# Kernel tuning notes

Measured on AMD Instinct MI355X. Metric: run time of the kernel, lower is better.

Reference implementation:

```python
import jax, jax.numpy as jnp
import numpy as np

N = 50000   # nodes (subjects in population graph)
E = 800000  # edges (similarity graph, avg degree 16)
F = 128     # node features


def setup_inputs() -> dict:
    key = jax.random.key(0)
    ks = jax.random.split(key, 8)

    def glorot(k, shape):
        scale = 1.0 / np.sqrt(shape[0])
        return jax.random.normal(k, shape, jnp.float32) * scale

    x = jax.random.normal(ks[0], (N, F), jnp.float32)
    edge_index = jax.random.randint(ks[1], (2, E), 0, N, dtype=jnp.int64)
    return {
        "x": x,
        "edge_index": edge_index,
        "W1": glorot(ks[2], (F, 128)),   "b1": jnp.zeros((128,), jnp.float32),
        "W2": glorot(ks[3], (128, 64)),  "b2": jnp.zeros((64,), jnp.float32),
        "Wf1": glorot(ks[4], (64, 32)),  "bf1": jnp.zeros((32,), jnp.float32),
        "Wf2": glorot(ks[5], (32, 1)),   "bf2": jnp.zeros((1,), jnp.float32),
    }


def reference(x, edge_index, W1, b1, W2, b2, Wf1, bf1, Wf2, bf2):
    n = x.shape[0]
    # GCNConv (PyG default): add self-loops, symmetric deg^{-1/2} normalization
    loops = jnp.arange(n, dtype=edge_index.dtype)
    src = jnp.concatenate([edge_index[0], loops])  # [E+N]
    dst = jnp.concatenate([edge_index[1], loops])  # [E+N]
    deg = jax.ops.segment_sum(jnp.ones_like(dst, x.dtype), dst, num_segments=n)
    dinv = deg ** -0.5  # deg >= 1 thanks to self-loops
    norm = (dinv[src] * dinv[dst])[:, None]  # [E+N, 1]

    def gcn_conv(h, W, b):
        h = h @ W                                    # transform [n, out]
        msg = h[src] * norm                          # gather + normalize
        agg = jax.ops.segment_sum(msg, dst, num_segments=n)  # scatter-add
        return agg + b

    h = jnp.tanh(gcn_conv(x, W1, b1))
    h = jnp.tanh(gcn_conv(h, W2, b2))
    h = jnp.tanh(h @ Wf1 + bf1)
    return h @ Wf2 + bf2  # [n, 1] brain-age prediction
```

## Files before the change

### kernel.cpp

```cpp
#include <hip/hip_runtime.h>
#include <hip/hip_fp16.h>
#include <math.h>

#define TPB 256
#define CAP 64

typedef int   nt_i4 __attribute__((ext_vector_type(4)));
typedef unsigned nt_u4 __attribute__((ext_vector_type(4)));
typedef _Float16 f16x8 __attribute__((ext_vector_type(8)));
typedef float f32x4 __attribute__((ext_vector_type(4)));

__global__ __launch_bounds__(TPB) void init_degi(const int* __restrict__ e,
                                                 int* __restrict__ flag,
                                                 int* __restrict__ degi, int n) {
  int i = blockIdx.x * TPB + threadIdx.x;
  const int stride = gridDim.x * TPB;
  for (; i < n; i += stride) degi[i] = 0;
  if (blockIdx.x == 0) {
    __shared__ int found;
    if (threadIdx.x == 0) found = 0;
    __syncthreads();
    int nz = 0;
    for (int k = threadIdx.x; k < 2048; k += TPB)
      nz |= (e[2 * k + 1] != 0) ? 1 : 0;
    if (nz) atomicOr(&found, 1);
    __syncthreads();
    if (threadIdx.x == 0) *flag = found;
  }
}

__device__ __forceinline__ void load_edge(const void* eptr, int flag, int E,
                                          int e, int& s, int& d) {
  if (flag) {
    const int* p = (const int*)eptr;
    s = p[e];
    d = p[E + e];
  } else {
    const long long* p = (const long long*)eptr;
    s = (int)p[e];
    d = (int)p[E + e];
  }
}

__global__ __launch_bounds__(TPB) void build_ell(const void* __restrict__ eptr,
                                                 const int* __restrict__ flag,
                                                 int* __restrict__ degi,
                                                 int* __restrict__ ell, int E) {
  const int fl = *flag;
  const int t4 = (blockIdx.x * TPB + threadIdx.x) * 4;
  const int stride = gridDim.x * TPB * 4;
  for (int e0 = t4; e0 < E; e0 += stride) {
    if (e0 + 4 <= E) {
      int s[4], d[4];
      if (fl) {
        const int* p = (const int*)eptr;
        nt_i4 sv = __builtin_nontemporal_load((const nt_i4*)&p[e0]);
        nt_i4 dv = __builtin_nontemporal_load((const nt_i4*)&p[E + e0]);
        s[0] = sv.x; s[1] = sv.y; s[2] = sv.z; s[3] = sv.w;
        d[0] = dv.x; d[1] = dv.y; d[2] = dv.z; d[3] = dv.w;
      } else {
        const long long* p = (const long long*)eptr;
        nt_i4 sa = __builtin_nontemporal_load((const nt_i4*)&p[e0]);
        nt_i4 sb = __builtin_nontemporal_load((const nt_i4*)&p[e0 + 2]);
        nt_i4 da = __builtin_nontemporal_load((const nt_i4*)&p[E + e0]);
        nt_i4 db = __builtin_nontemporal_load((const nt_i4*)&p[E + e0 + 2]);
        s[0] = sa.x; s[1] = sa.z; s[2] = sb.x; s[3] = sb.z;
        d[0] = da.x; d[1] = da.z; d[2] = db.x; d[3] = db.z;
      }
#pragma unroll
      for (int j = 0; j < 4; j++) {
        int slot = atomicAdd(&degi[d[j]], 1);
        if (slot < CAP)
          __builtin_nontemporal_store(s[j], &ell[(size_t)d[j] * CAP + slot]);
      }
    } else {
      for (int e = e0; e < E; e++) {
        int s, d;
        load_edge(eptr, fl, E, e, s, d);
        int slot = atomicAdd(&degi[d], 1);
        if (slot < CAP)
          __builtin_nontemporal_store(s, &ell[(size_t)d * CAP + slot]);
      }
    }
  }
}

template <int NC, typename AT>
__global__ __launch_bounds__(TPB, 4) void gemm_mfma(const AT* __restrict__ A,
                                                    const float* __restrict__ W,
                                                    const int* __restrict__ degi,
                                                    __half* __restrict__ out, int nrows) {
  constexpr int K = 128;
  constexpr int WT = 136;
  constexpr int NT = NC / 16;
  __shared__ _Float16 Wt[NC * WT];

  const int tid = threadIdx.x;

  for (int idx = tid; idx < NC * (K / 2); idx += TPB) {
    int c = idx % NC;
    int p = idx / NC;
    float w0 = W[(2 * p) * NC + c];
    float w1 = W[(2 * p + 1) * NC + c];
    __half2* dst = (__half2*)&Wt[c * WT + 2 * p];
    *dst = __floats2half2_rn(w0, w1);
  }
  __syncthreads();

  const int w = tid >> 6;
  const int lane = tid & 63;
  const int l15 = lane & 15;
  const int q = lane >> 4;
  const int m_base = blockIdx.x * 64 + w * 16;
  const int m = m_base + l15;
  const bool mok = m < nrows;

  f32x4 acc[NT];
#pragma unroll
  for (int t = 0; t < NT; t++) acc[t] = (f32x4){0.f, 0.f, 0.f, 0.f};

#pragma unroll
  for (int ks = 0; ks < 4; ks++) {
    const int k0 = ks * 32;
    f16x8 a;
    if (sizeof(AT) == 4) {
      float4 f0 = make_float4(0.f, 0.f, 0.f, 0.f), f1 = f0;
      if (mok) {
        const float* ap = (const float*)A + (size_t)m * K + k0 + q * 8;
        f0 = *(const float4*)ap;
        f1 = *(const float4*)(ap + 4);
      }
      a[0] = (_Float16)f0.x; a[1] = (_Float16)f0.y;
      a[2] = (_Float16)f0.z; a[3] = (_Float16)f0.w;
      a[4] = (_Float16)f1.x; a[5] = (_Float16)f1.y;
      a[6] = (_Float16)f1.z; a[7] = (_Float16)f1.w;
    } else {
      union { uint4 u; f16x8 h; } ld;
      ld.u = make_uint4(0, 0, 0, 0);
      if (mok)
        ld.u = *(const uint4*)((const __half*)A + (size_t)m * K + k0 + q * 8);
      a = ld.h;
    }
#pragma unroll
    for (int t = 0; t < NT; t++) {
      f16x8 b = *(const f16x8*)&Wt[(t * 16 + l15) * WT + k0 + q * 8];
      acc[t] = __builtin_amdgcn_mfma_f32_16x16x32_f16(a, b, acc[t], 0, 0, 0);
    }
  }

#pragma unroll
  for (int r = 0; r < 4; r++) {
    int row = m_base + q * 4 + r;
    if (row >= nrows) continue;
    float di = rsqrtf((float)(degi[row] + 1));
#pragma unroll
    for (int t = 0; t < NT; t++)
      out[(size_t)row * NC + t * 16 + l15] = (__half)(acc[t][r] * di);
  }
}

__global__ __launch_bounds__(TPB) void gcn_agg1_fused(const int* __restrict__ degi,
                                                      const int* __restrict__ ell,
                                                      const __half* __restrict__ t,
                                                      const float* __restrict__ bias,
                                                      const float* __restrict__ W2,
                                                      __half* __restrict__ t2, int n) {
  constexpr int NC = 128, LPN = 16, CPL = 8, NPB = TPB / LPN;
  constexpr int WT = 136;
  __shared__ _Float16 Wt2[64 * WT];
  __shared__ _Float16 Ah[NPB * WT];

  const int tid = threadIdx.x;

  for (int idx = tid; idx < 64 * 64; idx += TPB) {
    int c = idx & 63;
    int p = idx >> 6;
    float w0 = W2[(2 * p) * 64 + c];
    float w1 = W2[(2 * p + 1) * 64 + c];
    *(__half2*)&Wt2[c * WT + 2 * p] = __floats2half2_rn(w0, w1);
  }

  const int g = tid / LPN;
  const int ll = tid % LPN;
  const int node = blockIdx.x * NPB + g;
  const bool active = node < n;

  if (active) {
    int dg = degi[node];
    float di = rsqrtf((float)(dg + 1));
    int deg = dg > CAP ? CAP : dg;
    const int* nbr = &ell[(size_t)node * CAP];
    const __half* tp = t + (size_t)ll * CPL;

    float acc[CPL];
#pragma unroll
    for (int c = 0; c < CPL; c++) acc[c] = 0.f;

    union Ld { uint4 u4; __half2 h[4]; };
    auto addv = [&](const Ld& v) {
#pragma unroll
      for (int c = 0; c < 4; c++) {
        float2 f = __half22float2(v.h[c]);
        acc[2 * c] += f.x;
        acc[2 * c + 1] += f.y;
      }
    };

    int j = 0;
    for (; j + 8 <= deg; j += 8) {
      nt_i4 n0 = __builtin_nontemporal_load((const nt_i4*)&nbr[j]);
      nt_i4 n1 = __builtin_nontemporal_load((const nt_i4*)&nbr[j + 4]);
      Ld v0, v1, v2, v3, v4, v5, v6, v7;
      v0.u4 = *(const uint4*)&tp[(size_t)n0.x * NC];
      v1.u4 = *(const uint4*)&tp[(size_t)n0.y * NC];
      v2.u4 = *(const uint4*)&tp[(size_t)n0.z * NC];
      v3.u4 = *(const uint4*)&tp[(size_t)n0.w * NC];
      v4.u4 = *(const uint4*)&tp[(size_t)n1.x * NC];
      v5.u4 = *(const uint4*)&tp[(size_t)n1.y * NC];
      v6.u4 = *(const uint4*)&tp[(size_t)n1.z * NC];
      v7.u4 = *(const uint4*)&tp[(size_t)n1.w * NC];
      addv(v0); addv(v1); addv(v2); addv(v3);
      addv(v4); addv(v5); addv(v6); addv(v7);
    }
    for (; j + 4 <= deg; j += 4) {
      nt_i4 n0 = __builtin_nontemporal_load((const nt_i4*)&nbr[j]);
      Ld v0, v1, v2, v3;
      v0.u4 = *(const uint4*)&tp[(size_t)n0.x * NC];
      v1.u4 = *(const uint4*)&tp[(size_t)n0.y * NC];
      v2.u4 = *(const uint4*)&tp[(size_t)n0.z * NC];
      v3.u4 = *(const uint4*)&tp[(size_t)n0.w * NC];
      addv(v0); addv(v1); addv(v2); addv(v3);
    }
    for (; j < deg; j++) {
      Ld v;
      v.u4 = *(const uint4*)&tp[(size_t)nbr[j] * NC];
      addv(v);
    }
    {
      Ld v;
      v.u4 = *(const uint4*)&tp[(size_t)node * NC];
      addv(v);
    }

    const float* bp = &bias[ll * CPL];
    float bv[CPL];
#pragma unroll
    for (int c = 0; c < CPL; c += 4) {
      float4 b = *(const float4*)&bp[c];
      bv[c] = b.x; bv[c + 1] = b.y; bv[c + 2] = b.z; bv[c + 3] = b.w;
    }
    union { _Float16 h[8]; f16x8 v; } o;
#pragma unroll
    for (int c = 0; c < CPL; c++)
      o.h[c] = (_Float16)tanhf(acc[c] * di + bv[c]);
    *(f16x8*)&Ah[g * WT + ll * CPL] = o.v;
  }
  __syncthreads();

  const int w = tid >> 6;
  const int lane = tid & 63;
  const int l15 = lane & 15;
  const int q = lane >> 4;
  f32x4 acc2 = (f32x4){0.f, 0.f, 0.f, 0.f};
#pragma unroll
  for (int ks = 0; ks < 4; ks++) {
    f16x8 a = *(const f16x8*)&Ah[l15 * WT + ks * 32 + q * 8];
    f16x8 b = *(const f16x8*)&Wt2[(w * 16 + l15) * WT + ks * 32 + q * 8];
    acc2 = __builtin_amdgcn_mfma_f32_16x16x32_f16(a, b, acc2, 0, 0, 0);
  }
#pragma unroll
  for (int r = 0; r < 4; r++) {
    int rn = blockIdx.x * NPB + q * 4 + r;
    if (rn < n) {
      float d2 = rsqrtf((float)(degi[rn] + 1));
      t2[(size_t)rn * 64 + w * 16 + l15] = (__half)(acc2[r] * d2);
    }
  }
}

__global__ __launch_bounds__(TPB) void gcn_aggregate_head(
    const int* __restrict__ degi, const int* __restrict__ ell,
    const __half* __restrict__ t, const float* __restrict__ b2,
    const float* __restrict__ Wf1, const float* __restrict__ bf1,
    const float* __restrict__ Wf2, const float* __restrict__ bf2,
    float* __restrict__ out, int n) {
  constexpr int NC = 64, LPN = 16, NPB = TPB / LPN;
  __shared__ float hrow[NPB][68];
  __shared__ float Wf1s[64 * 32];
  __shared__ float Wf2s[32];
  const int tid = threadIdx.x;

#pragma unroll
  for (int i = 0; i < 2; i++) {
    int lid = tid + i * TPB;
    *(float4*)&Wf1s[lid * 4] = *(const float4*)&Wf1[lid * 4];
  }
  if (tid < 32) Wf2s[tid] = Wf2[tid];

  const int g = tid / LPN;
  const int ll = tid % LPN;
  const int node = blockIdx.x * NPB + g;
  const bool active = node < n;

  float acc[4] = {0.f, 0.f, 0.f, 0.f};
  if (active) {
    int dg = degi[node];
    float di = rsqrtf((float)(dg + 1));
    int deg = dg > CAP ? CAP : dg;
    const int* nbr = &ell[(size_t)node * CAP];
    const __half* tp = t + (size_t)ll * 4;
    union Ld { uint2 u2; __half2 h[2]; };
    auto addv = [&](const Ld& v) {
      float2 f0 = __half22float2(v.h[0]);
      float2 f1 = __half22float2(v.h[1]);
      acc[0] += f0.x; acc[1] += f0.y; acc[2] += f1.x; acc[3] += f1.y;
    };
    int j = 0;
    for (; j + 8 <= deg; j += 8) {
      nt_i4 n0 = __builtin_nontemporal_load((const nt_i4*)&nbr[j]);
      nt_i4 n1 = __builtin_nontemporal_load((const nt_i4*)&nbr[j + 4]);
      Ld v0, v1, v2, v3, v4, v5, v6, v7;
      v0.u2 = *(const uint2*)&tp[(size_t)n0.x * NC];
      v1.u2 = *(const uint2*)&tp[(size_t)n0.y * NC];
      v2.u2 = *(const uint2*)&tp[(size_t)n0.z * NC];
      v3.u2 = *(const uint2*)&tp[(size_t)n0.w * NC];
      v4.u2 = *(const uint2*)&tp[(size_t)n1.x * NC];
      v5.u2 = *(const uint2*)&tp[(size_t)n1.y * NC];
      v6.u2 = *(const uint2*)&tp[(size_t)n1.z * NC];
      v7.u2 = *(const uint2*)&tp[(size_t)n1.w * NC];
      addv(v0); addv(v1); addv(v2); addv(v3);
      addv(v4); addv(v5); addv(v6); addv(v7);
    }
    for (; j + 4 <= deg; j += 4) {
      nt_i4 nn = __builtin_nontemporal_load((const nt_i4*)&nbr[j]);
      Ld v0, v1, v2, v3;
      v0.u2 = *(const uint2*)&tp[(size_t)nn.x * NC];
      v1.u2 = *(const uint2*)&tp[(size_t)nn.y * NC];
      v2.u2 = *(const uint2*)&tp[(size_t)nn.z * NC];
      v3.u2 = *(const uint2*)&tp[(size_t)nn.w * NC];
      addv(v0); addv(v1); addv(v2); addv(v3);
    }
    for (; j < deg; j++) {
      Ld v;
      v.u2 = *(const uint2*)&tp[(size_t)nbr[j] * NC];
      addv(v);
    }
    {
      Ld v;
      v.u2 = *(const uint2*)&tp[(size_t)node * NC];
      addv(v);
    }
    float4 b = *(const float4*)&b2[ll * 4];
    hrow[g][ll * 4 + 0] = tanhf(acc[0] * di + b.x);
    hrow[g][ll * 4 + 1] = tanhf(acc[1] * di + b.y);
    hrow[g][ll * 4 + 2] = tanhf(acc[2] * di + b.z);
    hrow[g][ll * 4 + 3] = tanhf(acc[3] * di + b.w);
  }
  __syncthreads();

  float hid0 = bf1[ll];
  float hid1 = bf1[ll + 16];
#pragma unroll 8
  for (int i = 0; i < 64; i++) {
    float hv = hrow[g][i];
    hid0 += hv * Wf1s[i * 32 + ll];
    hid1 += hv * Wf1s[i * 32 + ll + 16];
  }
  float p = tanhf(hid0) * Wf2s[ll] + tanhf(hid1) * Wf2s[ll + 16];
  p += __shfl_down(p, 8, 16);
  p += __shfl_down(p, 4, 16);
  p += __shfl_down(p, 2, 16);
  p += __shfl_down(p, 1, 16);
  if (active && ll == 0) out[node] = p + bf2[0];
}

extern "C" void kernel_launch(void* const* d_in, const int* in_sizes, int n_in,
                              void* d_out, int out_size, void* d_ws, size_t ws_size,
                              hipStream_t stream) {
  const float* x   = (const float*)d_in[0];
  const void*  eix = d_in[1];
  const float* W1  = (const float*)d_in[2];
  const float* b1  = (const float*)d_in[3];
  const float* W2  = (const float*)d_in[4];
  const float* b2  = (const float*)d_in[5];
  const float* Wf1 = (const float*)d_in[6];
  const float* bf1 = (const float*)d_in[7];
  const float* Wf2 = (const float*)d_in[8];
  const float* bf2 = (const float*)d_in[9];
  float* out = (float*)d_out;

  const int N = in_sizes[0] / 128;
  const int E = in_sizes[1] / 2;

  char* ws = (char*)d_ws;
  size_t off = 0;
  int* degi = (int*)(ws + off); off += (size_t)N * 4;
  int* flag = (int*)(ws + off); off += 64;
  off = (off + 15) & ~(size_t)15;
  int* ell = (int*)(ws + off); off += (size_t)N * CAP * 4;
  off = (off + 15) & ~(size_t)15;
  __half* t1 = (__half*)(ws + off); off += (size_t)N * 128 * 2;
  __half* t2 = (__half*)(ws + off); off += (size_t)N * 64 * 2;
  (void)ws_size; (void)n_in; (void)out_size;

  init_degi<<<64, TPB, 0, stream>>>((const int*)eix, flag, degi, N);
  const int bblocks = (E + TPB * 4 - 1) / (TPB * 4);
  build_ell<<<bblocks, TPB, 0, stream>>>(eix, flag, degi, ell, E);

  gemm_mfma<128, float><<<(N + 63) / 64, TPB, 0, stream>>>(x, W1, degi, t1, N);

  gcn_agg1_fused<<<(N + 15) / 16, TPB, 0, stream>>>(degi, ell, t1, b1, W2, t2, N);

  gcn_aggregate_head<<<(N + 15) / 16, TPB, 0, stream>>>(degi, ell, t2, b2,
                                                        Wf1, bf1, Wf2, bf2, out, N);
}
```

Before: 232.9 us.

## Build ELL adjacency via two-pass bucketed counting sort instead of global atomics

Replaces the single-pass ELL build, which did a global atomicAdd per edge on scattered degree counters, with a two-phase binning scheme. Edges are first histogrammed per 128-node bucket in LDS and written as packed (dst,src) pairs into per-bucket regions. A second kernel then assigns ELL slots using LDS atomics per bucket. This aims to cut contended, scattered global atomics and random writes, at the cost of an extra pass over the edges, an intermediate pair buffer, and a fixed per-bucket capacity (BCAP) that silently drops edges if a bucket overflows.

```diff
diff --git a/kernel.cpp b/kernel.cpp
--- a/kernel.cpp
+++ b/kernel.cpp
@@ -4,29 +4,29 @@
 
 #define TPB 256
 #define CAP 64
+#define BSHIFT 7
+#define BSPAN 128
+#define NBLK 512
+#define BCAP 3072
 
 typedef int   nt_i4 __attribute__((ext_vector_type(4)));
 typedef unsigned nt_u4 __attribute__((ext_vector_type(4)));
 typedef _Float16 f16x8 __attribute__((ext_vector_type(8)));
 typedef float f32x4 __attribute__((ext_vector_type(4)));
 
-__global__ __launch_bounds__(TPB) void init_degi(const int* __restrict__ e,
-                                                 int* __restrict__ flag,
-                                                 int* __restrict__ degi, int n) {
-  int i = blockIdx.x * TPB + threadIdx.x;
-  const int stride = gridDim.x * TPB;
-  for (; i < n; i += stride) degi[i] = 0;
-  if (blockIdx.x == 0) {
-    __shared__ int found;
-    if (threadIdx.x == 0) found = 0;
-    __syncthreads();
-    int nz = 0;
-    for (int k = threadIdx.x; k < 2048; k += TPB)
-      nz |= (e[2 * k + 1] != 0) ? 1 : 0;
-    if (nz) atomicOr(&found, 1);
-    __syncthreads();
-    if (threadIdx.x == 0) *flag = found;
-  }
+__global__ __launch_bounds__(TPB) void init_pre(const int* __restrict__ e,
+                                                int* __restrict__ flag,
+                                                int* __restrict__ gcur, int nbuck) {
+  __shared__ int found;
+  if (threadIdx.x == 0) found = 0;
+  __syncthreads();
+  for (int b = threadIdx.x; b < nbuck; b += TPB) gcur[b] = 0;
+  int nz = 0;
+  for (int k = threadIdx.x; k < 2048; k += TPB)
+    nz |= (e[2 * k + 1] != 0) ? 1 : 0;
+  if (nz) atomicOr(&found, 1);
+  __syncthreads();
+  if (threadIdx.x == 0) *flag = found;
 }
 
 __device__ __forceinline__ void load_edge(const void* eptr, int flag, int E,
@@ -42,46 +42,110 @@
   }
 }
 
-__global__ __launch_bounds__(TPB) void build_ell(const void* __restrict__ eptr,
-                                                 const int* __restrict__ flag,
-                                                 int* __restrict__ degi,
-                                                 int* __restrict__ ell, int E) {
+__device__ __forceinline__ void load_edge4(const void* eptr, int flag, int E,
+                                           int e0, int* s, int* d) {
+  if (flag) {
+    const int* p = (const int*)eptr;
+    nt_i4 sv = __builtin_nontemporal_load((const nt_i4*)&p[e0]);
+    nt_i4 dv = __builtin_nontemporal_load((const nt_i4*)&p[E + e0]);
+    s[0] = sv.x; s[1] = sv.y; s[2] = sv.z; s[3] = sv.w;
+    d[0] = dv.x; d[1] = dv.y; d[2] = dv.z; d[3] = dv.w;
+  } else {
+    const long long* p = (const long long*)eptr;
+    nt_i4 sa = __builtin_nontemporal_load((const nt_i4*)&p[e0]);
+    nt_i4 sb = __builtin_nontemporal_load((const nt_i4*)&p[e0 + 2]);
+    nt_i4 da = __builtin_nontemporal_load((const nt_i4*)&p[E + e0]);
+    nt_i4 db = __builtin_nontemporal_load((const nt_i4*)&p[E + e0 + 2]);
+    s[0] = sa.x; s[1] = sa.z; s[2] = sb.x; s[3] = sb.z;
+    d[0] = da.x; d[1] = da.z; d[2] = db.x; d[3] = db.z;
+  }
+}
+
+__global__ __launch_bounds__(TPB) void bucket_pairs(const void* __restrict__ eptr,
+                                                    const int* __restrict__ flag,
+                                                    int* __restrict__ gcur,
+                                                    unsigned long long* __restrict__ pairs,
+                                                    int E, int nbuck, int chunk) {
+  extern __shared__ int lds[];
+  int* hist = lds;
+  int* cur = lds + nbuck;
+  const int tid = threadIdx.x;
   const int fl = *flag;
-  const int t4 = (blockIdx.x * TPB + threadIdx.x) * 4;
-  const int stride = gridDim.x * TPB * 4;
-  for (int e0 = t4; e0 < E; e0 += stride) {
-    if (e0 + 4 <= E) {
+  for (int b = tid; b < nbuck; b += TPB) hist[b] = 0;
+  __syncthreads();
+
+  const int start = blockIdx.x * chunk;
+  const int end = min(E, start + chunk);
+
+  for (int e0 = start + tid * 4; e0 < end; e0 += TPB * 4) {
+    if (e0 + 4 <= end) {
       int s[4], d[4];
-      if (fl) {
-        const int* p = (const int*)eptr;
-        nt_i4 sv = __builtin_nontemporal_load((const nt_i4*)&p[e0]);
-        nt_i4 dv = __builtin_nontemporal_load((const nt_i4*)&p[E + e0]);
-        s[0] = sv.x; s[1] = sv.y; s[2] = sv.z; s[3] = sv.w;
-        d[0] = dv.x; d[1] = dv.y; d[2] = dv.z; d[3] = dv.w;
-      } else {
-        const long long* p = (const long long*)eptr;
-        nt_i4 sa = __builtin_nontemporal_load((const nt_i4*)&p[e0]);
-        nt_i4 sb = __builtin_nontemporal_load((const nt_i4*)&p[e0 + 2]);
-        nt_i4 da = __builtin_nontemporal_load((const nt_i4*)&p[E + e0]);
-        nt_i4 db = __builtin_nontemporal_load((const nt_i4*)&p[E + e0 + 2]);
-        s[0] = sa.x; s[1] = sa.z; s[2] = sb.x; s[3] = sb.z;
-        d[0] = da.x; d[1] = da.z; d[2] = db.x; d[3] = db.z;
+      load_edge4(eptr, fl, E, e0, s, d);
+#pragma unroll
+      for (int j = 0; j < 4; j++) atomicAdd(&hist[d[j] >> BSHIFT], 1);
+    } else {
+      for (int e = e0; e < end; e++) {
+        int s, d;
+        load_edge(eptr, fl, E, e, s, d);
+        atomicAdd(&hist[d >> BSHIFT], 1);
       }
+    }
+  }
+  __syncthreads();
+
+  for (int b = tid; b < nbuck; b += TPB) {
+    int c = hist[b];
+    cur[b] = (c > 0) ? (b * BCAP + atomicAdd(&gcur[b], c)) : 0;
+  }
+  __syncthreads();
+
+  for (int e0 = start + tid * 4; e0 < end; e0 += TPB * 4) {
+    if (e0 + 4 <= end) {
+      int s[4], d[4];
+      load_edge4(eptr, fl, E, e0, s, d);
 #pragma unroll
       for (int j = 0; j < 4; j++) {
-        int slot = atomicAdd(&degi[d[j]], 1);
-        if (slot < CAP)
-          __builtin_nontemporal_store(s[j], &ell[(size_t)d[j] * CAP + slot]);
+        int slot = atomicAdd(&cur[d[j] >> BSHIFT], 1);
+        unsigned long long pv =
+            ((unsigned long long)(unsigned)d[j] << 32) | (unsigned)s[j];
+        __builtin_nontemporal_store(pv, &pairs[slot]);
       }
     } else {
-      for (int e = e0; e < E; e++) {
+      for (int e = e0; e < end; e++) {
         int s, d;
         load_edge(eptr, fl, E, e, s, d);
-        int slot = atomicAdd(&degi[d], 1);
-        if (slot < CAP)
-          __builtin_nontemporal_store(s, &ell[(size_t)d * CAP + slot]);
+        int slot = atomicAdd(&cur[d >> BSHIFT], 1);
+        unsigned long long pv =
+            ((unsigned long long)(unsigned)d << 32) | (unsigned)s;
+        __builtin_nontemporal_store(pv, &pairs[slot]);
       }
     }
+  }
+}
+
+__global__ __launch_bounds__(TPB) void ell_from_pairs(const unsigned long long* __restrict__ pairs,
+                                                      const int* __restrict__ gcur,
+                                                      int* __restrict__ ell,
+                                                      int* __restrict__ degi, int n) {
+  __shared__ int cnt[BSPAN];
+  const int b = blockIdx.x;
+  const int tid = threadIdx.x;
+  const int base = b << BSHIFT;
+  for (int j = tid; j < BSPAN; j += TPB) cnt[j] = 0;
+  __syncthreads();
+  const int npair = min(gcur[b], BCAP);
+  const unsigned long long* pp = &pairs[(size_t)b * BCAP];
+  for (int i = tid; i < npair; i += TPB) {
+    unsigned long long pr = __builtin_nontemporal_load(&pp[i]);
+    int d = (int)(pr >> 32);
+    int s = (int)(unsigned)pr;
+    int slot = atomicAdd(&cnt[d - base], 1);
+    if (slot < CAP) ell[(size_t)d * CAP + slot] = s;
+  }
+  __syncthreads();
+  for (int j = tid; j < BSPAN; j += TPB) {
+    int node = base + j;
+    if (node < n) degi[node] = cnt[j];
   }
 }
 
@@ -391,21 +455,28 @@
 
   const int N = in_sizes[0] / 128;
   const int E = in_sizes[1] / 2;
+  const int nbuck = (N + BSPAN - 1) >> BSHIFT;
+  int chunk = (E + NBLK - 1) / NBLK;
+  chunk = (chunk + 3) & ~3;
+  const size_t ldsBytes = (size_t)nbuck * 2 * 4;
 
   char* ws = (char*)d_ws;
   size_t off = 0;
   int* degi = (int*)(ws + off); off += (size_t)N * 4;
   int* flag = (int*)(ws + off); off += 64;
+  int* gcur = (int*)(ws + off); off += (size_t)(nbuck + 16) * 4;
   off = (off + 15) & ~(size_t)15;
+  unsigned long long* pairs = (unsigned long long*)(ws + off);
+  off += (size_t)nbuck * BCAP * 8;
   int* ell = (int*)(ws + off); off += (size_t)N * CAP * 4;
   off = (off + 15) & ~(size_t)15;
   __half* t1 = (__half*)(ws + off); off += (size_t)N * 128 * 2;
   __half* t2 = (__half*)(ws + off); off += (size_t)N * 64 * 2;
   (void)ws_size; (void)n_in; (void)out_size;
 
-  init_degi<<<64, TPB, 0, stream>>>((const int*)eix, flag, degi, N);
-  const int bblocks = (E + TPB * 4 - 1) / (TPB * 4);
-  build_ell<<<bblocks, TPB, 0, stream>>>(eix, flag, degi, ell, E);
+  init_pre<<<1, TPB, 0, stream>>>((const int*)eix, flag, gcur, nbuck);
+  bucket_pairs<<<NBLK, TPB, ldsBytes, stream>>>(eix, flag, gcur, pairs, E, nbuck, chunk);
+  ell_from_pairs<<<nbuck, TPB, 0, stream>>>(pairs, gcur, ell, degi, N);
 
   gemm_mfma<128, float><<<(N + 63) / 64, TPB, 0, stream>>>(x, W1, degi, t1, N);
 
```

After: 227.7 us. -2.2%, faster.
